# Kernel tuning notes

Hardware: AMD Instinct MI355X
Metric: run time of the kernel (lower is better)

## Reference

```python
import jax, jax.numpy as jnp
import numpy as np

B, C, H, W = 32, 384, 56, 56  # batch, channels, spatial; meta_kernel_size == H


def setup_inputs() -> dict:
    key = jax.random.key(0)
    k1, k2, k3 = jax.random.split(key, 3)
    x = jax.random.normal(k1, (B, C, H, W), dtype=jnp.float32)
    # depthwise conv weight: [dim, 1, meta_kernel_size, 1] (OIHW, I = in_ch/groups = 1)
    weight = jax.random.normal(k2, (C, 1, H, 1), dtype=jnp.float32) * 0.02
    bias = jax.random.normal(k3, (C,), dtype=jnp.float32)
    return {"x": x, "weight": weight, "bias": bias}


def reference(x, weight, bias):
    # circular padding along H: cat(x, x[:, :, :-1, :]) -> [B, C, 2H-1, W]
    x_cat = jnp.concatenate([x, x[:, :, :-1, :]], axis=2)
    # depthwise (groups = C) valid conv with full-height kernel -> [B, C, H, W]
    out = jax.lax.conv_general_dilated(
        x_cat, weight,
        window_strides=(1, 1), padding='VALID',
        dimension_numbers=('NCHW', 'OIHW', 'NCHW'),
        feature_group_count=x.shape[1],
    )
    return out + bias[None, :, None, None]
```

## Files before the change

### kernel.cpp

```cpp
#include <hip/hip_runtime.h>

#define NB 32
#define NC 384
#define NH 56
#define NW 56
#define HP 64

typedef __attribute__((ext_vector_type(8))) short  bf16x8;
typedef __attribute__((ext_vector_type(4))) float  f32x4;

__device__ __forceinline__ unsigned short f2bf(float f) {
    unsigned u = __float_as_uint(f);
    return (unsigned short)((u + 0x7FFFu + ((u >> 16) & 1u)) >> 16);
}

__global__ __launch_bounds__(256, 3) void gcc_Conv2d_64347200028713_kernel(
    const float* __restrict__ x,
    const float* __restrict__ wgt,
    const float* __restrict__ bias,
    float* __restrict__ out)
{
    const int tid  = threadIdx.x;
    const int lane = tid & 63;
    const int wave = tid >> 6;
    const int c    = blockIdx.x >> 3;
    const int g    = blockIdx.x & 7;
    const int b    = g * 4 + wave;
    const size_t plane = (size_t)(b * NC + c);

    __shared__ float wsh[NH];
    __shared__ __align__(16) unsigned short Mw[HP * HP];

    if (tid < NH) wsh[tid] = wgt[c * NH + tid];
    __syncthreads();
#pragma unroll
    for (int i = tid; i < HP * HP; i += 256) {
        const int h = i >> 6, j = i & 63;
        unsigned short v = 0;
        if (h < NH && j < NH) { int d = j - h; if (d < 0) d += NH; v = f2bf(wsh[d]); }
        Mw[(h << 6) | (j ^ ((h & 7) << 3))] = v;
    }
    __syncthreads();

    const int l15 = lane & 15;
    const int kg  = lane >> 4;
    const float* __restrict__ xp = x   + plane * (NH * NW);
    float*       __restrict__ op = out + plane * (NH * NW);
    const float bc = bias[c];

    bf16x8 af[4][2];
#pragma unroll
    for (int ht = 0; ht < 4; ++ht) {
        const int row = ht * 16 + l15;
#pragma unroll
        for (int kk = 0; kk < 2; ++kk) {
            const int idx = (row << 6) | ((kk * 32 + kg * 8) ^ ((row & 7) << 3));
            af[ht][kk] = *reinterpret_cast<const bf16x8*>(&Mw[idx]);
        }
    }

#pragma unroll
    for (int half = 0; half < 2; ++half) {
        f32x4 acc[4][2] = {};
#pragma unroll
        for (int kk = 0; kk < 2; ++kk) {
            int j0 = kk * 32 + kg * 8;
            if (j0 > 48) j0 = 48;
            bf16x8 bf[2];
#pragma unroll
            for (int wtl = 0; wtl < 2; ++wtl) {
                int n = (half * 2 + wtl) * 16 + l15;
                if (n > 55) n = 55;
                const float* bp = xp + j0 * NW + n;
#pragma unroll
                for (int e = 0; e < 8; ++e)
                    bf[wtl][e] = (short)f2bf(bp[e * NW]);
            }
#pragma unroll
            for (int ht = 0; ht < 4; ++ht) {
#pragma unroll
                for (int wtl = 0; wtl < 2; ++wtl)
                    acc[ht][wtl] = __builtin_amdgcn_mfma_f32_16x16x32_bf16(
                        af[ht][kk], bf[wtl], acc[ht][wtl], 0, 0, 0);
            }
        }
#pragma unroll
        for (int ht = 0; ht < 4; ++ht) {
#pragma unroll
            for (int wtl = 0; wtl < 2; ++wtl) {
                const int ww = (half * 2 + wtl) * 16 + l15;
                if (ww < NW) {
#pragma unroll
                    for (int r = 0; r < 4; ++r) {
                        const int hh = ht * 16 + kg * 4 + r;
                        if (hh < NH)
                            op[hh * NW + ww] = acc[ht][wtl][r] + bc;
                    }
                }
            }
        }
    }
}

extern "C" void kernel_launch(void* const* d_in, const int* in_sizes, int n_in,
                              void* d_out, int out_size, void* d_ws, size_t ws_size,
                              hipStream_t stream)
{
    const float* x    = (const float*)d_in[0];
    const float* wgt  = (const float*)d_in[1];
    const float* bias = (const float*)d_in[2];
    float* out        = (float*)d_out;

    const int grid  = NC * 8;
    const int block = 256;

    gcc_Conv2d_64347200028713_kernel<<<grid, block, 0, stream>>>(x, wgt, bias, out);
}
```

Before: 341.3 us.

## Stage input plane in LDS via coalesced float4 loads and transpose

Each wave now loads its whole 56x56 input plane with coalesced float4 global loads issued before the weight-matrix setup. It converts the data to bf16 and writes it transposed into a padded per-wave LDS tile. The MFMA B operands then come from single 16-byte LDS reads instead of eight strided scalar global loads per fragment, and the XOR swizzle on the weight matrix is replaced by a row padding of 72. The cost is about 36KB more shared memory per block, which may limit occupancy below the requested 3 blocks per CU.

```diff
diff --git a/kernel.cpp b/kernel.cpp
--- a/kernel.cpp
+++ b/kernel.cpp
@@ -5,9 +5,11 @@
 #define NH 56
 #define NW 56
 #define HP 64
+#define XR 72
 
 typedef __attribute__((ext_vector_type(8))) short  bf16x8;
 typedef __attribute__((ext_vector_type(4))) float  f32x4;
+typedef __attribute__((ext_vector_type(4))) unsigned int u32x4;
 
 __device__ __forceinline__ unsigned short f2bf(float f) {
     unsigned u = __float_as_uint(f);
@@ -29,7 +31,21 @@
     const size_t plane = (size_t)(b * NC + c);
 
     __shared__ float wsh[NH];
-    __shared__ __align__(16) unsigned short Mw[HP * HP];
+    __shared__ __align__(16) unsigned short Mw[HP * XR];
+    __shared__ __align__(16) unsigned short Xt_all[4][HP * XR];
+
+    const float* __restrict__ xp = x + plane * (NH * NW);
+
+    const int ls  = (lane < 56) ? lane : 55;
+    const int wq  = ls % 14;
+    const int jin = ls / 14;
+    float4 va[7], vb[7];
+#pragma unroll
+    for (int it = 0; it < 7; ++it) {
+        const int j0 = it * 8 + jin * 2;
+        va[it] = *reinterpret_cast<const float4*>(xp + j0 * NW + wq * 4);
+        vb[it] = *reinterpret_cast<const float4*>(xp + (j0 + 1) * NW + wq * 4);
+    }
 
     if (tid < NH) wsh[tid] = wgt[c * NH + tid];
     __syncthreads();
@@ -38,54 +54,63 @@
         const int h = i >> 6, j = i & 63;
         unsigned short v = 0;
         if (h < NH && j < NH) { int d = j - h; if (d < 0) d += NH; v = f2bf(wsh[d]); }
-        Mw[(h << 6) | (j ^ ((h & 7) << 3))] = v;
+        Mw[h * XR + j] = v;
     }
     __syncthreads();
 
+    unsigned short* Xt = Xt_all[wave];
+    {
+        u32x4 z = {0u, 0u, 0u, 0u};
+        *reinterpret_cast<u32x4*>(&Xt[lane * XR + 56]) = z;
+    }
+    if (lane < 56) {
+#pragma unroll
+        for (int it = 0; it < 7; ++it) {
+            const int j0 = it * 8 + jin * 2;
+#pragma unroll
+            for (int i = 0; i < 4; ++i) {
+                const float a = (&va[it].x)[i];
+                const float bv = (&vb[it].x)[i];
+                const unsigned p = (unsigned)f2bf(a) | ((unsigned)f2bf(bv) << 16);
+                *reinterpret_cast<unsigned*>(&Xt[(wq * 4 + i) * XR + j0]) = p;
+            }
+        }
+    }
+
     const int l15 = lane & 15;
     const int kg  = lane >> 4;
-    const float* __restrict__ xp = x   + plane * (NH * NW);
-    float*       __restrict__ op = out + plane * (NH * NW);
     const float bc = bias[c];
+    float* __restrict__ op = out + plane * (NH * NW);
 
     bf16x8 af[4][2];
 #pragma unroll
-    for (int ht = 0; ht < 4; ++ht) {
-        const int row = ht * 16 + l15;
+    for (int ht = 0; ht < 4; ++ht)
 #pragma unroll
-        for (int kk = 0; kk < 2; ++kk) {
-            const int idx = (row << 6) | ((kk * 32 + kg * 8) ^ ((row & 7) << 3));
-            af[ht][kk] = *reinterpret_cast<const bf16x8*>(&Mw[idx]);
-        }
-    }
+        for (int kk = 0; kk < 2; ++kk)
+            af[ht][kk] = *reinterpret_cast<const bf16x8*>(
+                &Mw[(ht * 16 + l15) * XR + kk * 32 + kg * 8]);
 
 #pragma unroll
     for (int half = 0; half < 2; ++half) {
         f32x4 acc[4][2] = {};
 #pragma unroll
         for (int kk = 0; kk < 2; ++kk) {
-            int j0 = kk * 32 + kg * 8;
-            if (j0 > 48) j0 = 48;
-            bf16x8 bf[2];
+            bf16x8 bfr[2];
 #pragma unroll
             for (int wtl = 0; wtl < 2; ++wtl) {
-                int n = (half * 2 + wtl) * 16 + l15;
-                if (n > 55) n = 55;
-                const float* bp = xp + j0 * NW + n;
-#pragma unroll
-                for (int e = 0; e < 8; ++e)
-                    bf[wtl][e] = (short)f2bf(bp[e * NW]);
+                const int n = (half * 2 + wtl) * 16 + l15;
+                bfr[wtl] = *reinterpret_cast<const bf16x8*>(
+                    &Xt[n * XR + kk * 32 + kg * 8]);
             }
 #pragma unroll
-            for (int ht = 0; ht < 4; ++ht) {
+            for (int ht = 0; ht < 4; ++ht)
 #pragma unroll
                 for (int wtl = 0; wtl < 2; ++wtl)
                     acc[ht][wtl] = __builtin_amdgcn_mfma_f32_16x16x32_bf16(
-                        af[ht][kk], bf[wtl], acc[ht][wtl], 0, 0, 0);
-            }
+                        af[ht][kk], bfr[wtl], acc[ht][wtl], 0, 0, 0);
         }
 #pragma unroll
-        for (int ht = 0; ht < 4; ++ht) {
+        for (int ht = 0; ht < 4; ++ht)
 #pragma unroll
             for (int wtl = 0; wtl < 2; ++wtl) {
                 const int ww = (half * 2 + wtl) * 16 + l15;
@@ -98,7 +123,6 @@
                     }
                 }
             }
-        }
     }
 }
 
```

Result: faster. 299.5 us (-12.3%).
